# Optimization experiments

Measured on AMD Instinct MI355X. Metric: run time of the kernel, lower is better.

Reference implementation:

```python
import jax, jax.numpy as jnp
import numpy as np

SCORE_THRESH = 0.05
IOU_THRESH = 0.5
TOP_K = 1000      # candidates fed to NMS
MAX_DET = 100     # padded output detections


def _build_anchors(H, W):
    """Standard RetinaNet anchors: levels P3..P7, 3 ratios x 3 scales."""
    ratios = np.array([0.5, 1.0, 2.0])
    scales = np.array([2 ** 0, 2 ** (1.0 / 3.0), 2 ** (2.0 / 3.0)])
    all_anchors = []
    for lvl in [3, 4, 5, 6, 7]:
        stride = 2 ** lvl
        base_size = 2 ** (lvl + 2)
        # 9 base anchors centered at origin (ratio-major, scale-minor ordering)
        s = base_size * np.tile(scales, len(ratios))          # [9]
        r = np.repeat(ratios, len(scales))                    # [9]
        areas = s * s
        w = np.sqrt(areas / r)
        h = w * r
        base = np.stack([-w / 2, -h / 2, w / 2, h / 2], axis=1)  # [9,4]
        fh = (H + stride - 1) // stride
        fw = (W + stride - 1) // stride
        sx = (np.arange(fw) + 0.5) * stride
        sy = (np.arange(fh) + 0.5) * stride
        gx, gy = np.meshgrid(sx, sy)
        shifts = np.stack([gx.ravel(), gy.ravel(), gx.ravel(), gy.ravel()], axis=1)  # [fh*fw,4]
        all_anchors.append((shifts[:, None, :] + base[None, :, :]).reshape(-1, 4))
    return np.concatenate(all_anchors, axis=0).astype(np.float32)  # [A,4]


def setup_inputs() -> dict:
    key = jax.random.key(0)
    k1, k2 = jax.random.split(key)
    H = W = 1024
    C = 80
    anchors = jnp.asarray(_build_anchors(H, W))[None]            # [1,A,4]
    A = anchors.shape[1]
    classifications = jax.random.uniform(k1, (1, A, C), dtype=jnp.float32)
    regressions = jax.random.normal(k2, (1, A, 4), dtype=jnp.float32)
    return {"classifications": classifications, "regressions": regressions,
            "anchors": anchors, "img_h": H, "img_w": W}


def _decode_clip(anchors, regressions, img_h, img_w):
    # BBoxTransform with mean 0, std [0.1,0.1,0.2,0.2]
    aw = anchors[..., 2] - anchors[..., 0]
    ah = anchors[..., 3] - anchors[..., 1]
    acx = anchors[..., 0] + 0.5 * aw
    acy = anchors[..., 1] + 0.5 * ah
    dx = regressions[..., 0] * 0.1
    dy = regressions[..., 1] * 0.1
    dw = regressions[..., 2] * 0.2
    dh = regressions[..., 3] * 0.2
    pcx = acx + dx * aw
    pcy = acy + dy * ah
    pw = jnp.exp(dw) * aw
    ph = jnp.exp(dh) * ah
    boxes = jnp.stack([pcx - 0.5 * pw, pcy - 0.5 * ph,
                       pcx + 0.5 * pw, pcy + 0.5 * ph], axis=-1)
    # ClipBoxes
    lo = jnp.zeros(4, boxes.dtype)
    hi = jnp.array([img_w, img_h, img_w, img_h], boxes.dtype)
    return jnp.clip(boxes, lo, hi)  # [1,A,4]


def _nms_keep(boxes, valid):
    """Sequential greedy NMS over score-sorted boxes [K,4]; returns keep mask [K]."""
    K = boxes.shape[0]
    areas = jnp.maximum(boxes[:, 2] - boxes[:, 0], 0) * jnp.maximum(boxes[:, 3] - boxes[:, 1], 0)
    idx = jnp.arange(K)

    def body(i, keep):
        b = boxes[i]
        xx1 = jnp.maximum(b[0], boxes[:, 0])
        yy1 = jnp.maximum(b[1], boxes[:, 1])
        xx2 = jnp.minimum(b[2], boxes[:, 2])
        yy2 = jnp.minimum(b[3], boxes[:, 3])
        inter = jnp.maximum(xx2 - xx1, 0) * jnp.maximum(yy2 - yy1, 0)
        iou = inter / (areas[i] + areas - inter + 1e-8)
        suppress = (iou > IOU_THRESH) & (idx > i)
        return jnp.where(keep[i], keep & ~suppress, keep)

    return jax.lax.fori_loop(0, K, body, valid)


def reference(classifications, regressions, anchors, img_h, img_w):
    boxes = _decode_clip(anchors, regressions, img_h, img_w)       # [1,A,4]
    scores = jnp.max(classifications, axis=2)                      # [1,A]
    # Score threshold: mask out low scores, keep fixed shape (padded NMS)
    s0 = jnp.where(scores[0] > SCORE_THRESH, scores[0], -1.0)      # [A]
    top_scores, top_idx = jax.lax.top_k(s0, TOP_K)                 # sorted desc
    cand_boxes = boxes[0, top_idx]                                 # [K,4]
    keep = _nms_keep(cand_boxes, top_scores > SCORE_THRESH)        # [K]
    final = jnp.where(keep, top_scores, -1.0)
    det_scores, sel = jax.lax.top_k(final, MAX_DET)                # [100]
    det_idx = top_idx[sel]                                         # indices into A
    det_valid = det_scores > SCORE_THRESH
    cls = classifications[0, det_idx]                              # [100,C]
    nms_scores = jnp.where(det_valid, jnp.max(cls, axis=1), 0.0)
    nms_class = jnp.where(det_valid, jnp.argmax(cls, axis=1), -1)
    det_boxes = jnp.where(det_valid[:, None], boxes[0, det_idx], 0.0)
    return (nms_scores, nms_class, det_boxes)
```

## Files before the change

### kernel.cpp

```cpp
#include <hip/hip_runtime.h>
#include <stdint.h>

#define SCORE_THRESH 0.05f
#define IOU_THRESH 0.5f
#define TOP_K 1000
#define MAX_DET 100

#define D0_BITS 13
#define D0_BINS 8192
#define NREP 8
#define CAND_CAP 2048
#define NMS_CHUNK 128

typedef unsigned int u32;
typedef unsigned long long u64;

#define OFF_HIST0    0
#define OFF_HIST1    262144
#define OFF_STATE    524288
#define OFF_BAR      525312
#define MEMSET_LEN   553984
#define OFF_CAND     553984
#define OFF_RFLAG    562176
#define OFF_SIDX     566176
#define OFF_SSCORE   570176
#define OFF_CBOX     574176
#define OFF_M        590176
#define OFF_SCORES   718176

#define BAR_STRIDE_U32 1024

__device__ __forceinline__ u32 order_f32(float f) {
    u32 b = __float_as_uint(f);
    return (b & 0x80000000u) ? ~b : (b | 0x80000000u);
}

__device__ __forceinline__ void st_sc(u32* p, u32 v)   { __hip_atomic_store(p, v, __ATOMIC_RELAXED, __HIP_MEMORY_SCOPE_AGENT); }
__device__ __forceinline__ void st_sc(float* p, float v){ __hip_atomic_store(p, v, __ATOMIC_RELAXED, __HIP_MEMORY_SCOPE_AGENT); }
__device__ __forceinline__ void st_sc(u64* p, u64 v)   { __hip_atomic_store(p, v, __ATOMIC_RELAXED, __HIP_MEMORY_SCOPE_AGENT); }
__device__ __forceinline__ u32  ld_sc(u32* p)          { return __hip_atomic_load(p, __ATOMIC_RELAXED, __HIP_MEMORY_SCOPE_AGENT); }

__device__ __forceinline__ void gbar(u32* barr, int k, int b, u32 gsz, bool dowait) {
    __syncthreads();
    if (threadIdx.x == 0) {
        asm volatile("s_waitcnt vmcnt(0)" ::: "memory");
        u32* base = barr + (size_t)k * BAR_STRIDE_U32;
        int g = b & 7;
        if (__hip_atomic_fetch_add(base + g * 32, 1u, __ATOMIC_RELAXED,
                                   __HIP_MEMORY_SCOPE_AGENT) == gsz - 1u)
            __hip_atomic_fetch_add(base + 8 * 32, 1u, __ATOMIC_RELAXED,
                                   __HIP_MEMORY_SCOPE_AGENT);
        if (dowait) {
            while (ld_sc(base + 8 * 32) < 8u)
                __builtin_amdgcn_s_sleep(8);
        }
        asm volatile("" ::: "memory");
    }
    __syncthreads();
}

union ShMem {
    u32 hl[D0_BINS / 2];
    u32 wtot[4];
    struct { u32 wcnt[4]; u32 wbase[4]; u32 bbase; } cmp;
    struct { u64 ckeys[8]; u32 wpart[4][8]; } rank;
    struct {
        u64 Ml[2 * NMS_CHUNK * 16];
        u64 keepS[16];
        u32 nib[256];
        int act[TOP_K];
        u32 wsum[4];
        int nactS;
        int det[MAX_DET];
    } nms;
};

__global__ void __launch_bounds__(256, 2)
mega(const float* __restrict__ cls, const float* __restrict__ regs,
     const float* __restrict__ anchors, const int* __restrict__ pH,
     const int* __restrict__ pW, int A, int C,
     char* __restrict__ ws, float* __restrict__ out)
{
    __shared__ ShMem sh;
    u32*   hist0  = (u32*)(ws + OFF_HIST0);
    u32*   hist1  = (u32*)(ws + OFF_HIST1);
    u32*   state  = (u32*)(ws + OFF_STATE);
    u32*   barr   = (u32*)(ws + OFF_BAR);
    u32*   cand   = (u32*)(ws + OFF_CAND);
    u32*   rflag  = (u32*)(ws + OFF_RFLAG);
    u32*   sidx   = (u32*)(ws + OFF_SIDX);
    float* sscore = (float*)(ws + OFF_SSCORE);
    float* cbox   = (float*)(ws + OFF_CBOX);
    u64*   M      = (u64*)(ws + OFF_M);
    float* scores = (float*)(ws + OFF_SCORES);

    const int t = threadIdx.x;
    const int b = blockIdx.x;
    const int G = gridDim.x;
    const int gid = b * 256 + t;
    const int gstride = G * 256;
    const int lane = t & 63, wv = t >> 6;
    const u32 gsz = (u32)(G >> 3);

    if (C == 80) {
        for (int i = t; i < D0_BINS / 2; i += 256) sh.hl[i] = 0;
        __syncthreads();
        int sub = t & 3;
        int la  = t >> 2;
        int nstrips = (A + 63) >> 6;
        int per = (nstrips + G - 1) / G;
        for (int s = 0; s < per; s++) {
            int a = (b * per + s) * 64 + la;
            float m = -1e30f;
            if (a < A) {
                const float* p = cls + (size_t)a * 80 + sub * 4;
                #pragma unroll
                for (int k2 = 0; k2 < 5; k2++) {
                    float4 v = *(const float4*)(p + k2 * 16);
                    m = fmaxf(m, fmaxf(fmaxf(v.x, v.y), fmaxf(v.z, v.w)));
                }
            }
            m = fmaxf(m, __shfl_xor(m, 1, 64));
            m = fmaxf(m, __shfl_xor(m, 2, 64));
            if (sub == 0 && a < A) {
                float s0 = (m > SCORE_THRESH) ? m : -1.0f;
                st_sc(&scores[a], s0);
                u32 d = order_f32(s0) >> (32 - D0_BITS);
                atomicAdd(&sh.hl[d >> 1], (d & 1) ? 0x10000u : 1u);
            }
        }
        __syncthreads();
        u32* rep = hist0 + (size_t)(b & (NREP - 1)) * D0_BINS;
        for (int i = t; i < D0_BINS / 2; i += 256) {
            u32 v = sh.hl[i];
            if (v & 0xFFFFu) atomicAdd(&rep[2 * i],     v & 0xFFFFu);
            if (v >> 16)     atomicAdd(&rep[2 * i + 1], v >> 16);
        }
    } else {
        u32* rep = hist0 + (size_t)(b & (NREP - 1)) * D0_BINS;
        for (int a = gid; a < A; a += gstride) {
            const float* p = cls + (size_t)a * C;
            float m = -1e30f;
            for (int c = 0; c < C; c++) m = fmaxf(m, p[c]);
            float s0 = (m > SCORE_THRESH) ? m : -1.0f;
            st_sc(&scores[a], s0);
            atomicAdd(&rep[order_f32(s0) >> (32 - D0_BITS)], 1u);
        }
    }
    gbar(barr, 0, b, gsz, true);

    if (b == 0) {
        u32 cnt[32];
        #pragma unroll
        for (int i = 0; i < 32; i++) cnt[i] = 0;
        const uint4* hp = (const uint4*)hist0;
        #pragma unroll
        for (int r = 0; r < NREP; r++) {
            #pragma unroll
            for (int i = 0; i < 8; i++) {
                uint4 v = hp[r * (D0_BINS / 4) + t * 8 + i];
                cnt[4*i]   += v.x; cnt[4*i+1] += v.y;
                cnt[4*i+2] += v.z; cnt[4*i+3] += v.w;
            }
        }
        u32 s = 0;
        #pragma unroll
        for (int i = 0; i < 32; i++) s += cnt[i];
        u32 x = s;
        for (int off = 1; off < 64; off <<= 1) {
            u32 v = (u32)__shfl_down((int)x, off, 64);
            if (lane + off < 64) x += v;
        }
        if (lane == 0) sh.wtot[wv] = x;
        __syncthreads();
        u32 above = x - s;
        for (int w = wv + 1; w < 4; w++) above += sh.wtot[w];
        if (above < TOP_K && above + s >= TOP_K) {
            u32 cum = above;
            for (int i = 31; i >= 0; i--) {
                cum += cnt[i];
                if (cum >= TOP_K) {
                    st_sc(&state[1 * 32], (u32)(t * 32 + i));
                    st_sc(&state[0 * 32], TOP_K - (cum - cnt[i]));
                    break;
                }
            }
        }
    } else {
        float acc = 0.0f;
        for (int a = gid; a < A; a += gstride) acc += scores[a];
        asm volatile("" :: "v"(acc));
    }
    gbar(barr, 1, b, gsz, true);

    {
        u32 d0cut = state[1 * 32];
        for (int a = gid; a < A; a += gstride) {
            u32 key = order_f32(scores[a]);
            if ((key >> (32 - D0_BITS)) == d0cut)
                atomicAdd(&hist1[(key >> 3) & 0xFFFFu], 1u);
        }
    }
    gbar(barr, 2, b, gsz, b == 0);

    if (b == 0) {
        u32 k = state[0 * 32];
        const uint4* hp = (const uint4*)hist1;
        u32 chk[8]; u32 s = 0;
        #pragma unroll
        for (int c = 0; c < 8; c++) {
            u32 cs = 0;
            #pragma unroll
            for (int i = 0; i < 8; i++) {
                uint4 v = hp[t * 64 + c * 8 + i];
                cs += v.x + v.y + v.z + v.w;
            }
            chk[c] = cs; s += cs;
        }
        u32 x = s;
        for (int off = 1; off < 64; off <<= 1) {
            u32 v = (u32)__shfl_down((int)x, off, 64);
            if (lane + off < 64) x += v;
        }
        if (lane == 0) sh.wtot[wv] = x;
        __syncthreads();
        u32 above = x - s;
        for (int w = wv + 1; w < 4; w++) above += sh.wtot[w];
        if (above < k && above + s >= k) {
            u32 cum = above;
            bool done = false;
            for (int c = 7; c >= 0 && !done; c--) {
                if (cum + chk[c] >= k) {
                    for (int i = 7; i >= 0 && !done; i--) {
                        uint4 v = hp[t * 64 + c * 8 + i];
                        u32 vv[4] = {v.x, v.y, v.z, v.w};
                        for (int q = 3; q >= 0 && !done; q--) {
                            cum += vv[q];
                            if (cum >= k) {
                                st_sc(&state[2 * 32], (u32)(t * 256 + c * 32 + i * 4 + q));
                                done = true;
                            }
                        }
                    }
                } else cum += chk[c];
            }
        }
    }
    gbar(barr, 3, b, gsz, true);

    {
        u32 cut = (state[1 * 32] << 16) | state[2 * 32];
        int nr = (A + gstride - 1) / gstride;
        u32 mycnt = 0;
        for (int r = 0; r < nr; r++) {
            int a = gid + r * gstride;
            mycnt += ((a < A) && ((order_f32(scores[a]) >> 3) >= cut)) ? 1u : 0u;
        }
        u32 wc = mycnt;
        wc += (u32)__shfl_xor((int)wc, 1, 64);
        wc += (u32)__shfl_xor((int)wc, 2, 64);
        wc += (u32)__shfl_xor((int)wc, 4, 64);
        wc += (u32)__shfl_xor((int)wc, 8, 64);
        wc += (u32)__shfl_xor((int)wc, 16, 64);
        wc += (u32)__shfl_xor((int)wc, 32, 64);
        if (lane == 0) sh.cmp.wcnt[wv] = wc;
        __syncthreads();
        if (t == 0) {
            u32 s = 0;
            #pragma unroll
            for (int w = 0; w < 4; w++) { sh.cmp.wbase[w] = s; s += sh.cmp.wcnt[w]; }
            sh.cmp.bbase = s ? atomicAdd(&state[5 * 32], s) : 0u;
        }
        __syncthreads();
        u32 off = sh.cmp.bbase + sh.cmp.wbase[wv];
        for (int r = 0; r < nr; r++) {
            int a = gid + r * gstride;
            bool pass = (a < A) && ((order_f32(scores[a]) >> 3) >= cut);
            u64 mask = __ballot(pass ? 1 : 0);
            if (pass) {
                u32 pos = off + (u32)__popcll(mask & ((1ull << lane) - 1ull));
                if (pos < CAND_CAP) st_sc(&cand[pos], (u32)a);
            }
            off += (u32)__popcll(mask);
        }
    }
    gbar(barr, 4, b, gsz, b < CAND_CAP / 8);

    if (b < CAND_CAP / 8) {
        int n = (int)state[5 * 32]; if (n > CAND_CAP) n = CAND_CAP;
        u64 kj[8];
        #pragma unroll
        for (int q = 0; q < 8; q++) {
            int j = t * 8 + q;
            u64 kk = 0ull;
            if (j < n) {
                u32 a = cand[j];
                kk = ((u64)order_f32(scores[a]) << 32) | (u64)(0xFFFFFFFFu - a);
            }
            kj[q] = kk;
        }
        for (int bb = b; bb < CAND_CAP / 8; bb += G) {
            if (t < 8) {
                int c = bb * 8 + t;
                u64 ck = 0ull;
                if (c < n) {
                    u32 a = cand[c];
                    ck = ((u64)order_f32(scores[a]) << 32) | (u64)(0xFFFFFFFFu - a);
                }
                sh.rank.ckeys[t] = ck;
            }
            __syncthreads();
            u64 ck[8];
            #pragma unroll
            for (int q = 0; q < 8; q++) ck[q] = sh.rank.ckeys[q];
            u32 cnt8[8] = {0,0,0,0,0,0,0,0};
            #pragma unroll
            for (int q = 0; q < 8; q++) {
                u64 kq = kj[q];
                #pragma unroll
                for (int q2 = 0; q2 < 8; q2++) cnt8[q2] += (kq > ck[q2]) ? 1u : 0u;
            }
            #pragma unroll
            for (int q2 = 0; q2 < 8; q2++) {
                u32 x = cnt8[q2];
                x += (u32)__shfl_xor((int)x, 1, 64);
                x += (u32)__shfl_xor((int)x, 2, 64);
                x += (u32)__shfl_xor((int)x, 4, 64);
                x += (u32)__shfl_xor((int)x, 8, 64);
                x += (u32)__shfl_xor((int)x, 16, 64);
                x += (u32)__shfl_xor((int)x, 32, 64);
                if (lane == 0) sh.rank.wpart[wv][q2] = x;
            }
            __syncthreads();
            if (t < 8) {
                int c = bb * 8 + t;
                if (c < n) {
                    u32 rank = sh.rank.wpart[0][t] + sh.rank.wpart[1][t]
                             + sh.rank.wpart[2][t] + sh.rank.wpart[3][t];
                    if (rank < TOP_K) {
                        u32 a = cand[c];
                        st_sc(&sidx[rank], a);
                        st_sc(&sscore[rank], scores[a]);
                        float4 an = *(const float4*)(anchors + (size_t)a * 4);
                        float4 rg = *(const float4*)(regs + (size_t)a * 4);
                        float aw = an.z - an.x, ah = an.w - an.y;
                        float acx = an.x + 0.5f * aw, acy = an.y + 0.5f * ah;
                        float pcx = acx + (rg.x * 0.1f) * aw;
                        float pcy = acy + (rg.y * 0.1f) * ah;
                        float pw = expf(rg.z * 0.2f) * aw;
                        float ph = expf(rg.w * 0.2f) * ah;
                        float W = (float)(*pW), H = (float)(*pH);
                        st_sc(&cbox[rank * 4 + 0], fminf(fmaxf(pcx - 0.5f * pw, 0.0f), W));
                        st_sc(&cbox[rank * 4 + 1], fminf(fmaxf(pcy - 0.5f * ph, 0.0f), H));
                        st_sc(&cbox[rank * 4 + 2], fminf(fmaxf(pcx + 0.5f * pw, 0.0f), W));
                        st_sc(&cbox[rank * 4 + 3], fminf(fmaxf(pcy + 0.5f * ph, 0.0f), H));
                    }
                }
            }
            __syncthreads();
        }
    }
    gbar(barr, 5, b, gsz, b * 4 < TOP_K);

    {
        const float4* B4 = (const float4*)cbox;
        for (int i = b * 4 + wv; i < TOP_K; i += G * 4) {
            float4 bi = B4[i];
            float ai = fmaxf(bi.z - bi.x, 0.0f) * fmaxf(bi.w - bi.y, 0.0f);
            u64 any = 0ull;
            for (int w = 0; w < 16; w++) {
                int j = w * 64 + lane;
                bool sup = false;
                if (j < TOP_K && j > i) {
                    float4 bj = B4[j];
                    float aj = fmaxf(bj.z - bj.x, 0.0f) * fmaxf(bj.w - bj.y, 0.0f);
                    float xx1 = fmaxf(bi.x, bj.x), yy1 = fmaxf(bi.y, bj.y);
                    float xx2 = fminf(bi.z, bj.z), yy2 = fminf(bi.w, bj.w);
                    float inter = fmaxf(xx2 - xx1, 0.0f) * fmaxf(yy2 - yy1, 0.0f);
                    float iou = inter / (ai + aj - inter + 1e-8f);
                    sup = iou > IOU_THRESH;
                }
                u64 mask = __ballot(sup ? 1 : 0);
                if (lane == 0) { st_sc(&M[(size_t)i * 16 + w], mask); any |= mask; }
            }
            if (lane == 0) st_sc(&rflag[i], (any != 0ull) ? 1u : 0u);
        }
    }
    gbar(barr, 6, b, gsz, b == 0);

    if (b == 0) {
        {
            u32 nb = 0;
            int j0 = 4 * t;
            #pragma unroll
            for (int q = 0; q < 4; q++) {
                int j = j0 + q;
                if (j < TOP_K && sscore[j] > SCORE_THRESH) nb |= (1u << q);
            }
            sh.nms.nib[t] = nb;
        }
        u32 flags = 0; int cnt = 0;
        {
            int r0 = 4 * t;
            #pragma unroll
            for (int q = 0; q < 4; q++) {
                int r = r0 + q;
                if (r < TOP_K && rflag[r]) { flags |= (1u << q); cnt++; }
            }
        }
        int x = cnt;
        for (int off = 1; off < 64; off <<= 1) {
            int v = __shfl_up(x, off, 64);
            if (lane >= off) x += v;
        }
        if (lane == 63) sh.nms.wsum[wv] = (u32)x;
        __syncthreads();
        if (t < 16) {
            u64 w = 0;
            for (int m2 = 0; m2 < 16; m2++)
                w |= ((u64)sh.nms.nib[t * 16 + m2]) << (4 * m2);
            sh.nms.keepS[t] = w;
        }
        int base = 0;
        for (int w = 0; w < wv; w++) base += (int)sh.nms.wsum[w];
        int pos = base + x - cnt;
        {
            int r0 = 4 * t;
            #pragma unroll
            for (int q = 0; q < 4; q++)
                if (flags & (1u << q)) sh.nms.act[pos++] = r0 + q;
        }
        if (t == 0) {
            int na = 0;
            for (int w = 0; w < 4; w++) na += (int)sh.nms.wsum[w];
            sh.nms.nactS = na;
        }
        __syncthreads();
        int nact = sh.nms.nactS;
        int nchunks = (nact + NMS_CHUNK - 1) / NMS_CHUNK;

        if (nchunks > 0) {
            int cn0 = (nact < NMS_CHUNK) ? nact : NMS_CHUNK;
            for (int i = t; i < cn0 * 16; i += 256) {
                int row = sh.nms.act[i >> 4];
                sh.nms.Ml[i] = M[(size_t)row * 16 + (i & 15)];
            }
        }
        __syncthreads();
        u64 kp = (wv == 0 && lane < 16) ? sh.nms.keepS[lane] : 0ull;
        for (int ci = 0; ci < nchunks; ci++) {
            int c0 = ci * NMS_CHUNK;
            int cn = (nact - c0 < NMS_CHUNK) ? (nact - c0) : NMS_CHUNK;
            int cur = (ci & 1) * (NMS_CHUNK * 16);
            if (ci + 1 < nchunks && t >= 64) {
                int c0n = c0 + NMS_CHUNK;
                int cnn = (nact - c0n < NMS_CHUNK) ? (nact - c0n) : NMS_CHUNK;
                int nxt = ((ci + 1) & 1) * (NMS_CHUNK * 16);
                for (int i = t - 64; i < cnn * 16; i += 192) {
                    int row = sh.nms.act[c0n + (i >> 4)];
                    sh.nms.Ml[nxt + i] = M[(size_t)row * 16 + (i & 15)];
                }
            }
            if (wv == 0) {
                u64 mreg = (lane < 16 && cn > 0) ? sh.nms.Ml[cur + lane] : 0ull;
                for (int k = 0; k < cn; k++) {
                    u64 mnx = (lane < 16 && k + 1 < cn)
                            ? sh.nms.Ml[cur + (k + 1) * 16 + lane] : 0ull;
                    int i = sh.nms.act[c0 + k];
                    u64 kw = __shfl(kp, i >> 6, 64);
                    if ((kw >> (i & 63)) & 1ull) kp &= ~mreg;
                    mreg = mnx;
                }
            }
            __syncthreads();
        }
        if (wv == 0 && lane < 16) sh.nms.keepS[lane] = kp;
        __syncthreads();

        if (t == 0) {
            int cnt2 = 0;
            for (int w = 0; w < 16 && cnt2 < MAX_DET; w++) {
                u64 kw = sh.nms.keepS[w];
                while (kw && cnt2 < MAX_DET) {
                    int bbit = __ffsll((unsigned long long)kw) - 1;
                    sh.nms.det[cnt2++] = w * 64 + bbit;
                    kw &= kw - 1;
                }
            }
            for (; cnt2 < MAX_DET; cnt2++) sh.nms.det[cnt2] = -1;
        }
        __syncthreads();
        if (t < MAX_DET) {
            int i = sh.nms.det[t];
            if (i >= 0) {
                u32 a = sidx[i];
                const float* p = cls + (size_t)a * C;
                float best = -1e30f; int bc = 0;
                if (C == 80) {
                    #pragma unroll
                    for (int c4 = 0; c4 < 20; c4++) {
                        float4 v = *(const float4*)(p + c4 * 4);
                        if (v.x > best) { best = v.x; bc = c4 * 4; }
                        if (v.y > best) { best = v.y; bc = c4 * 4 + 1; }
                        if (v.z > best) { best = v.z; bc = c4 * 4 + 2; }
                        if (v.w > best) { best = v.w; bc = c4 * 4 + 3; }
                    }
                } else {
                    best = p[0]; bc = 0;
                    for (int c = 1; c < C; c++) {
                        float v = p[c];
                        if (v > best) { best = v; bc = c; }
                    }
                }
                out[t] = best;
                out[MAX_DET + t] = (float)bc;
                out[2 * MAX_DET + t * 4 + 0] = cbox[i * 4 + 0];
                out[2 * MAX_DET + t * 4 + 1] = cbox[i * 4 + 1];
                out[2 * MAX_DET + t * 4 + 2] = cbox[i * 4 + 2];
                out[2 * MAX_DET + t * 4 + 3] = cbox[i * 4 + 3];
            } else {
                out[t] = 0.0f;
                out[MAX_DET + t] = -1.0f;
                out[2 * MAX_DET + t * 4 + 0] = 0.0f;
                out[2 * MAX_DET + t * 4 + 1] = 0.0f;
                out[2 * MAX_DET + t * 4 + 2] = 0.0f;
                out[2 * MAX_DET + t * 4 + 3] = 0.0f;
            }
        }
    }
}

extern "C" void kernel_launch(void* const* d_in, const int* in_sizes, int n_in,
                              void* d_out, int out_size, void* d_ws, size_t ws_size,
                              hipStream_t stream) {
    (void)n_in; (void)out_size; (void)ws_size;
    const float* cls     = (const float*)d_in[0];
    const float* regs    = (const float*)d_in[1];
    const float* anchors = (const float*)d_in[2];
    const int*   pH      = (const int*)d_in[3];
    const int*   pW      = (const int*)d_in[4];
    int A = in_sizes[1] / 4;
    int C = in_sizes[0] / A;

    static int nCU = 0;
    if (nCU <= 0) {
        int dev = 0;
        hipGetDevice(&dev);
        hipDeviceGetAttribute(&nCU, hipDeviceAttributeMultiprocessorCount, dev);
        if (nCU <= 0) nCU = 256;
    }
    int G = (2 * nCU) & ~7;
    if (G < 8) G = 8;

    char* ws = (char*)d_ws;
    hipMemsetAsync(ws, 0, MEMSET_LEN, stream);
    mega<<<dim3(G), dim3(256), 0, stream>>>(cls, regs, anchors, pH, pW, A, C,
                                            ws, (float*)d_out);
}
```

Before: 181.0 us.

## Replace hierarchical atomic grid barrier with per-block flag array barrier

The grid barrier changes from two-level atomic counters polled by one thread to a per-block flag array. Each block writes its own flag, and waiting blocks have all threads poll the flags in parallel, combining them with __syncthreads_and. This removes the atomic contention and the serial chain of counter increments. The histogram replica count also drops from 8 to 4, which shrinks the memset and workspace, and the grid is capped at 512 blocks. The risks are more polling traffic from every thread of each waiting block and more atomic contention on the histogram with fewer replicas. The flag barrier also drops the explicit vmcnt wait and the trailing __syncthreads, so it relies on relaxed ordering.

```diff
diff --git a/kernel.cpp b/kernel.cpp
--- a/kernel.cpp
+++ b/kernel.cpp
@@ -8,7 +8,7 @@
 
 #define D0_BITS 13
 #define D0_BINS 8192
-#define NREP 8
+#define NREP 4
 #define CAND_CAP 2048
 #define NMS_CHUNK 128
 
@@ -16,19 +16,19 @@
 typedef unsigned long long u64;
 
 #define OFF_HIST0    0
-#define OFF_HIST1    262144
-#define OFF_STATE    524288
-#define OFF_BAR      525312
-#define MEMSET_LEN   553984
-#define OFF_CAND     553984
-#define OFF_RFLAG    562176
-#define OFF_SIDX     566176
-#define OFF_SSCORE   570176
-#define OFF_CBOX     574176
-#define OFF_M        590176
-#define OFF_SCORES   718176
-
-#define BAR_STRIDE_U32 1024
+#define OFF_HIST1    131072
+#define OFF_STATE    393216
+#define OFF_BAR      394240
+#define MEMSET_LEN   408576
+#define OFF_CAND     408576
+#define OFF_RFLAG    416768
+#define OFF_SIDX     420768
+#define OFF_SSCORE   424768
+#define OFF_CBOX     428768
+#define OFF_M        444768
+#define OFF_SCORES   572768
+
+#define BAR_STRIDE_U32 512
 
 __device__ __forceinline__ u32 order_f32(float f) {
     u32 b = __float_as_uint(f);
@@ -40,23 +40,19 @@
 __device__ __forceinline__ void st_sc(u64* p, u64 v)   { __hip_atomic_store(p, v, __ATOMIC_RELAXED, __HIP_MEMORY_SCOPE_AGENT); }
 __device__ __forceinline__ u32  ld_sc(u32* p)          { return __hip_atomic_load(p, __ATOMIC_RELAXED, __HIP_MEMORY_SCOPE_AGENT); }
 
-__device__ __forceinline__ void gbar(u32* barr, int k, int b, u32 gsz, bool dowait) {
+__device__ __forceinline__ void gbar(u32* barr, int k, int b, int G, bool dowait) {
     __syncthreads();
-    if (threadIdx.x == 0) {
-        asm volatile("s_waitcnt vmcnt(0)" ::: "memory");
-        u32* base = barr + (size_t)k * BAR_STRIDE_U32;
-        int g = b & 7;
-        if (__hip_atomic_fetch_add(base + g * 32, 1u, __ATOMIC_RELAXED,
-                                   __HIP_MEMORY_SCOPE_AGENT) == gsz - 1u)
-            __hip_atomic_fetch_add(base + 8 * 32, 1u, __ATOMIC_RELAXED,
-                                   __HIP_MEMORY_SCOPE_AGENT);
-        if (dowait) {
-            while (ld_sc(base + 8 * 32) < 8u)
-                __builtin_amdgcn_s_sleep(8);
+    u32* f = barr + (size_t)k * BAR_STRIDE_U32;
+    if (threadIdx.x == 0) st_sc(&f[b], 1u);
+    if (dowait) {
+        for (;;) {
+            int my = 1;
+            for (int i = (int)threadIdx.x; i < G; i += 256) my &= (int)ld_sc(&f[i]);
+            if (__syncthreads_and(my)) break;
+            __builtin_amdgcn_s_sleep(8);
         }
         asm volatile("" ::: "memory");
     }
-    __syncthreads();
 }
 
 union ShMem {
@@ -100,7 +96,6 @@
     const int gid = b * 256 + t;
     const int gstride = G * 256;
     const int lane = t & 63, wv = t >> 6;
-    const u32 gsz = (u32)(G >> 3);
 
     if (C == 80) {
         for (int i = t; i < D0_BINS / 2; i += 256) sh.hl[i] = 0;
@@ -147,7 +142,7 @@
             atomicAdd(&rep[order_f32(s0) >> (32 - D0_BITS)], 1u);
         }
     }
-    gbar(barr, 0, b, gsz, true);
+    gbar(barr, 0, b, G, true);
 
     if (b == 0) {
         u32 cnt[32];
@@ -191,7 +186,7 @@
         for (int a = gid; a < A; a += gstride) acc += scores[a];
         asm volatile("" :: "v"(acc));
     }
-    gbar(barr, 1, b, gsz, true);
+    gbar(barr, 1, b, G, true);
 
     {
         u32 d0cut = state[1 * 32];
@@ -201,7 +196,7 @@
                 atomicAdd(&hist1[(key >> 3) & 0xFFFFu], 1u);
         }
     }
-    gbar(barr, 2, b, gsz, b == 0);
+    gbar(barr, 2, b, G, b == 0);
 
     if (b == 0) {
         u32 k = state[0 * 32];
@@ -246,7 +241,7 @@
             }
         }
     }
-    gbar(barr, 3, b, gsz, true);
+    gbar(barr, 3, b, G, true);
 
     {
         u32 cut = (state[1 * 32] << 16) | state[2 * 32];
@@ -284,7 +279,7 @@
             off += (u32)__popcll(mask);
         }
     }
-    gbar(barr, 4, b, gsz, b < CAND_CAP / 8);
+    gbar(barr, 4, b, G, b < CAND_CAP / 8);
 
     if (b < CAND_CAP / 8) {
         int n = (int)state[5 * 32]; if (n > CAND_CAP) n = CAND_CAP;
@@ -360,7 +355,7 @@
             __syncthreads();
         }
     }
-    gbar(barr, 5, b, gsz, b * 4 < TOP_K);
+    gbar(barr, 5, b, G, b * 4 < TOP_K);
 
     {
         const float4* B4 = (const float4*)cbox;
@@ -386,7 +381,7 @@
             if (lane == 0) st_sc(&rflag[i], (any != 0ull) ? 1u : 0u);
         }
     }
-    gbar(barr, 6, b, gsz, b == 0);
+    gbar(barr, 6, b, G, b == 0);
 
     if (b == 0) {
         {
@@ -549,7 +544,8 @@
         hipDeviceGetAttribute(&nCU, hipDeviceAttributeMultiprocessorCount, dev);
         if (nCU <= 0) nCU = 256;
     }
-    int G = (2 * nCU) & ~7;
+    int G = 2 * nCU;
+    if (G > 512) G = 512;
     if (G < 8) G = 8;
 
     char* ws = (char*)d_ws;
```

After: 187.8 us. +3.7%, slower.

## Compute histogram cutoffs redundantly per block to drop two grid barriers

Applied to the files above, without the earlier changes.

Every block now scans the replicated level-0 histogram itself and keeps the cutoff in shared memory, so the grid-wide barrier after the single-block scan goes away. The second radix pass uses a coarser 12-bit histogram with 4 replicas, which every block also reduces redundantly, removing another grid barrier. The candidate threshold becomes coarser, so more ties can pass into the candidate list. All blocks also repeat the histogram reads, and the smaller workspace and halved replica count may raise atomic contention.

```diff
diff --git a/kernel.cpp b/kernel.cpp
--- a/kernel.cpp
+++ b/kernel.cpp
@@ -8,7 +8,9 @@
 
 #define D0_BITS 13
 #define D0_BINS 8192
-#define NREP 8
+#define D1_BITS 12
+#define D1_BINS 4096
+#define NREP 4
 #define CAND_CAP 2048
 #define NMS_CHUNK 128
 
@@ -16,17 +18,17 @@
 typedef unsigned long long u64;
 
 #define OFF_HIST0    0
-#define OFF_HIST1    262144
-#define OFF_STATE    524288
-#define OFF_BAR      525312
-#define MEMSET_LEN   553984
-#define OFF_CAND     553984
-#define OFF_RFLAG    562176
-#define OFF_SIDX     566176
-#define OFF_SSCORE   570176
-#define OFF_CBOX     574176
-#define OFF_M        590176
-#define OFF_SCORES   718176
+#define OFF_HIST1    131072
+#define OFF_STATE    196608
+#define OFF_BAR      197632
+#define MEMSET_LEN   218112
+#define OFF_CAND     218112
+#define OFF_RFLAG    226304
+#define OFF_SIDX     230304
+#define OFF_SSCORE   234304
+#define OFF_CBOX     238304
+#define OFF_M        254304
+#define OFF_SCORES   382304
 
 #define BAR_STRIDE_U32 1024
 
@@ -82,6 +84,7 @@
      char* __restrict__ ws, float* __restrict__ out)
 {
     __shared__ ShMem sh;
+    __shared__ u32 shcut[3];
     u32*   hist0  = (u32*)(ws + OFF_HIST0);
     u32*   hist1  = (u32*)(ws + OFF_HIST1);
     u32*   state  = (u32*)(ws + OFF_STATE);
@@ -149,7 +152,7 @@
     }
     gbar(barr, 0, b, gsz, true);
 
-    if (b == 0) {
+    {
         u32 cnt[32];
         #pragma unroll
         for (int i = 0; i < 32; i++) cnt[i] = 0;
@@ -180,43 +183,44 @@
             for (int i = 31; i >= 0; i--) {
                 cum += cnt[i];
                 if (cum >= TOP_K) {
-                    st_sc(&state[1 * 32], (u32)(t * 32 + i));
-                    st_sc(&state[0 * 32], TOP_K - (cum - cnt[i]));
+                    shcut[0] = (u32)(t * 32 + i);
+                    shcut[1] = TOP_K - (cum - cnt[i]);
                     break;
                 }
             }
         }
-    } else {
-        float acc = 0.0f;
-        for (int a = gid; a < A; a += gstride) acc += scores[a];
-        asm volatile("" :: "v"(acc));
-    }
-    gbar(barr, 1, b, gsz, true);
+        __syncthreads();
+    }
+    const u32 d0cut = shcut[0];
+    const u32 krem  = shcut[1];
 
     {
-        u32 d0cut = state[1 * 32];
+        u32* rep1 = hist1 + (size_t)(b & (NREP - 1)) * D1_BINS;
         for (int a = gid; a < A; a += gstride) {
             u32 key = order_f32(scores[a]);
             if ((key >> (32 - D0_BITS)) == d0cut)
-                atomicAdd(&hist1[(key >> 3) & 0xFFFFu], 1u);
-        }
-    }
-    gbar(barr, 2, b, gsz, b == 0);
-
-    if (b == 0) {
-        u32 k = state[0 * 32];
+                atomicAdd(&rep1[(key >> 7) & (D1_BINS - 1)], 1u);
+        }
+    }
+    gbar(barr, 1, b, gsz, true);
+
+    {
+        u32 cnt[16];
+        #pragma unroll
+        for (int i = 0; i < 16; i++) cnt[i] = 0;
         const uint4* hp = (const uint4*)hist1;
-        u32 chk[8]; u32 s = 0;
-        #pragma unroll
-        for (int c = 0; c < 8; c++) {
-            u32 cs = 0;
-            #pragma unroll
-            for (int i = 0; i < 8; i++) {
-                uint4 v = hp[t * 64 + c * 8 + i];
-                cs += v.x + v.y + v.z + v.w;
-            }
-            chk[c] = cs; s += cs;
-        }
+        #pragma unroll
+        for (int r = 0; r < NREP; r++) {
+            #pragma unroll
+            for (int i = 0; i < 4; i++) {
+                uint4 v = hp[r * (D1_BINS / 4) + t * 4 + i];
+                cnt[4*i]   += v.x; cnt[4*i+1] += v.y;
+                cnt[4*i+2] += v.z; cnt[4*i+3] += v.w;
+            }
+        }
+        u32 s = 0;
+        #pragma unroll
+        for (int i = 0; i < 16; i++) s += cnt[i];
         u32 x = s;
         for (int off = 1; off < 64; off <<= 1) {
             u32 v = (u32)__shfl_down((int)x, off, 64);
@@ -226,35 +230,23 @@
         __syncthreads();
         u32 above = x - s;
         for (int w = wv + 1; w < 4; w++) above += sh.wtot[w];
-        if (above < k && above + s >= k) {
+        if (above < krem && above + s >= krem) {
             u32 cum = above;
-            bool done = false;
-            for (int c = 7; c >= 0 && !done; c--) {
-                if (cum + chk[c] >= k) {
-                    for (int i = 7; i >= 0 && !done; i--) {
-                        uint4 v = hp[t * 64 + c * 8 + i];
-                        u32 vv[4] = {v.x, v.y, v.z, v.w};
-                        for (int q = 3; q >= 0 && !done; q--) {
-                            cum += vv[q];
-                            if (cum >= k) {
-                                st_sc(&state[2 * 32], (u32)(t * 256 + c * 32 + i * 4 + q));
-                                done = true;
-                            }
-                        }
-                    }
-                } else cum += chk[c];
-            }
-        }
-    }
-    gbar(barr, 3, b, gsz, true);
+            for (int i = 15; i >= 0; i--) {
+                cum += cnt[i];
+                if (cum >= krem) { shcut[2] = (u32)(t * 16 + i); break; }
+            }
+        }
+        __syncthreads();
+    }
+    const u32 cut25 = (d0cut << D1_BITS) | shcut[2];
 
     {
-        u32 cut = (state[1 * 32] << 16) | state[2 * 32];
         int nr = (A + gstride - 1) / gstride;
         u32 mycnt = 0;
         for (int r = 0; r < nr; r++) {
             int a = gid + r * gstride;
-            mycnt += ((a < A) && ((order_f32(scores[a]) >> 3) >= cut)) ? 1u : 0u;
+            mycnt += ((a < A) && ((order_f32(scores[a]) >> 7) >= cut25)) ? 1u : 0u;
         }
         u32 wc = mycnt;
         wc += (u32)__shfl_xor((int)wc, 1, 64);
@@ -275,7 +267,7 @@
         u32 off = sh.cmp.bbase + sh.cmp.wbase[wv];
         for (int r = 0; r < nr; r++) {
             int a = gid + r * gstride;
-            bool pass = (a < A) && ((order_f32(scores[a]) >> 3) >= cut);
+            bool pass = (a < A) && ((order_f32(scores[a]) >> 7) >= cut25);
             u64 mask = __ballot(pass ? 1 : 0);
             if (pass) {
                 u32 pos = off + (u32)__popcll(mask & ((1ull << lane) - 1ull));
@@ -284,7 +276,7 @@
             off += (u32)__popcll(mask);
         }
     }
-    gbar(barr, 4, b, gsz, b < CAND_CAP / 8);
+    gbar(barr, 2, b, gsz, b < CAND_CAP / 8);
 
     if (b < CAND_CAP / 8) {
         int n = (int)state[5 * 32]; if (n > CAND_CAP) n = CAND_CAP;
@@ -360,7 +352,7 @@
             __syncthreads();
         }
     }
-    gbar(barr, 5, b, gsz, b * 4 < TOP_K);
+    gbar(barr, 3, b, gsz, b * 4 < TOP_K);
 
     {
         const float4* B4 = (const float4*)cbox;
@@ -386,7 +378,7 @@
             if (lane == 0) st_sc(&rflag[i], (any != 0ull) ? 1u : 0u);
         }
     }
-    gbar(barr, 6, b, gsz, b == 0);
+    gbar(barr, 4, b, gsz, b == 0);
 
     if (b == 0) {
         {
```

Measured after the change: 169.3 us. -6.5%, faster.
